# Performance work log

Measured on AMD Instinct MI355X. Metric: run time of the kernel, lower is better.

Reference implementation:

```python
import jax, jax.numpy as jnp
import numpy as np

_R, _C = 64, 64
_N = _R * _C
_SEC_PER_A = 31556926.0
_K = 0.01        # sheet_conductivity
_ALPHA = 1.25    # sheet_flow_exp
_HR = 0.1        # bedrock_step_height
_LR = 2.0        # cavity_spacing
_A = 5e-25       # cavity_closure_coeff
_NEXP = 3        # Glen exponent


def _build_grid():
    idx = np.arange(_N).reshape(_R, _C)
    tail = np.concatenate([idx[:, :-1].ravel(), idx[:-1, :].ravel()]).astype(np.int32)
    head = np.concatenate([idx[:, 1:].ravel(), idx[1:, :].ravel()]).astype(np.int32)
    L = tail.size
    links_at_node = -np.ones((_N, 4), np.int32)
    adj = -np.ones((_N, 4), np.int32)
    cnt = np.zeros(_N, np.int32)
    for l in range(L):
        for a, b in ((tail[l], head[l]), (head[l], tail[l])):
            links_at_node[a, cnt[a]] = l
            adj[a, cnt[a]] = b
            cnt[a] += 1
    r, c = np.divmod(np.arange(_N), _C)
    status = ((r == 0) | (r == _R - 1) | (c == 0) | (c == _C - 1)).astype(np.int32)
    return tail, head, links_at_node, adj, status


def setup_inputs():
    key = jax.random.key(0)
    k = jax.random.split(key, 8)
    tail, head, links_at_node, adj, status = _build_grid()
    L = tail.size
    bedrock = jax.random.uniform(k[0], (_N,), jnp.float32, 0.0, 500.0)
    ice_thk = jax.random.uniform(k[1], (_N,), jnp.float32, 100.0, 1000.0)
    overburden = 917.0 * 9.81 * ice_thk
    base_potential = 1000.0 * 9.81 * bedrock + overburden
    potential = base_potential - 0.3 * overburden + 1e3 * jax.random.normal(k[2], (_N,), jnp.float32)
    sheet_thickness = jax.random.uniform(k[3], (_N,), jnp.float32, 0.01, 0.1)
    sliding_velocity = jax.random.uniform(k[4], (L,), jnp.float32, 10.0, 100.0)
    specific_melt_rate = jax.random.uniform(k[5], (_N,), jnp.float32, 1e-7, 1e-6)
    link_length = jnp.full((L,), 100.0, jnp.float32)
    adj_j = jnp.asarray(adj)
    # mean over ALL 4 slots, padded entries contribute 0 (matches original jnp.mean)
    adj_pot = jnp.mean(jnp.where(adj_j != -1, base_potential[adj_j], 0.0), axis=1)
    inflow = jnp.where(base_potential > adj_pot, 1, -1) * (jnp.asarray(status) > 0)
    return dict(
        base_potential=base_potential,
        overburden_pressure=overburden,
        specific_melt_rate=specific_melt_rate,
        sheet_thickness=sheet_thickness,
        potential=potential,
        sliding_velocity=sliding_velocity,
        link_length=link_length,
        link_tail=jnp.asarray(tail),
        link_head=jnp.asarray(head),
        links_at_node=jnp.asarray(links_at_node),
        inflow_outflow=inflow.astype(jnp.int32),
        dt=3600,
    )


def reference(base_potential, overburden_pressure, specific_melt_rate, sheet_thickness,
              potential, sliding_velocity, link_length, link_tail, link_head,
              links_at_node, inflow_outflow, dt):
    N = base_potential.shape[0]
    t, h = link_tail, link_head
    # --- elliptic operator assembly (per-link, scatter into dense [N,N]) ---
    sheets = 0.5 * (sheet_thickness[t] + sheet_thickness[h])
    inv_grad = jnp.abs((potential[t] - potential[h]) / link_length) ** (-0.5)
    c = -_K * sheets ** _ALPHA * link_length * inv_grad  # symmetric link coefficient (<0)
    dir_row = inflow_outflow == 1  # Dirichlet rows
    ct = jnp.where(dir_row[t], 0.0, c)  # contribution into row tail
    ch = jnp.where(dir_row[h], 0.0, c)  # contribution into row head
    M = (jnp.zeros((N, N), base_potential.dtype)
         .at[t, h].add(ct).at[h, t].add(ch)
         .at[t, t].add(-ct).at[h, h].add(-ch))
    M = jnp.where(dir_row[:, None], jnp.eye(N, dtype=M.dtype), M)
    forcing = jnp.where(dir_row, base_potential - overburden_pressure, specific_melt_rate)
    new_potential = jnp.linalg.solve(M, forcing)
    # --- sheet thickness: map_mean_of_links_to_node then Newton on node-local ODE ---
    valid = links_at_node != -1
    lv = (sliding_velocity / _SEC_PER_A)[links_at_node]  # [N,4]
    sliding = jnp.abs(jnp.sum(jnp.where(valid, lv, 0.0), axis=1)
                      / jnp.maximum(valid.sum(axis=1), 1))
    pressure = base_potential - new_potential
    dtf = jnp.asarray(dt, base_potential.dtype)
    # residual r(h) = h - h0 - dt*(sliding*(HR-h)/LR - A*P^n*h) is LINEAR in h,
    # so Newton converges in one exact step -> closed form:
    new_h = (sheet_thickness + dtf * sliding * _HR / _LR) / (
        1.0 + dtf * (sliding / _LR + _A * pressure ** _NEXP))
    return new_potential, new_h
```

## Files before the change

kernel.cpp:

```cpp
#include <hip/hip_runtime.h>
#include <math.h>


#define NT    512
#define NPT   8
#define NN    4096
#define NC    1024
#define NCC   256
#define CCIT  20
#define MAXIT 40

enum : int { RSHL1 = 0x101, RSHR1 = 0x111,
             ROR8 = 0x128, ROR12 = 0x12C, ROR14 = 0x12E, ROR15 = 0x12F,
             WSHL1 = 0x130, WSHR1 = 0x138 };

template<int CTRL>
__device__ __forceinline__ float dppf(float x) {
    return __int_as_float(__builtin_amdgcn_update_dpp(
        __float_as_int(x), __float_as_int(x), CTRL, 0xF, 0xF, false));
}
template<int CTRL>
__device__ __forceinline__ double dppd(double x) {
    const int lo = __double2loint(x), hi = __double2hiint(x);
    const int l2 = __builtin_amdgcn_update_dpp(lo, lo, CTRL, 0xF, 0xF, false);
    const int h2 = __builtin_amdgcn_update_dpp(hi, hi, CTRL, 0xF, 0xF, false);
    return __hiloint2double(h2, l2);
}
__device__ __forceinline__ void pl16sw(int& a, int& b) {
    asm volatile("s_nop 1\n\tv_permlane16_swap_b32 %0, %1" : "+v"(a), "+v"(b));
}
__device__ __forceinline__ void pl32sw(int& a, int& b) {
    asm volatile("s_nop 1\n\tv_permlane32_swap_b32 %0, %1" : "+v"(a), "+v"(b));
}
__device__ __forceinline__ float shift_dn16(float x, bool inR2) {
    int a = __float_as_int(x), b = __float_as_int(x);
    pl16sw(a, b);
    int g = b, g2 = b;
    pl32sw(g, g2);
    return __int_as_float(inR2 ? g : a);
}
__device__ __forceinline__ float shift_up16(float x, bool inR1) {
    int a = __float_as_int(x), b = __float_as_int(x);
    pl16sw(a, b);
    int d1 = __float_as_int(x), d2 = __float_as_int(x);
    pl32sw(d1, d2);
    int e1 = d2, e2 = d2;
    pl16sw(e1, e2);
    return __int_as_float(inR1 ? e1 : b);
}
__device__ __forceinline__ double dsw32(double x) {
    int lo = __double2loint(x), hi = __double2hiint(x);
    int a = lo, b = lo; pl32sw(a, b);
    int c = hi, d = hi; pl32sw(c, d);
    return __hiloint2double(d, b);
}
__device__ __forceinline__ double dsw16(double x) {
    int lo = __double2loint(x), hi = __double2hiint(x);
    int a = lo, b = lo; pl16sw(a, b);
    int c = hi, d = hi; pl16sw(c, d);
    return __hiloint2double(d, b);
}

__global__ __launch_bounds__(NT, 1)
void sds_solver(const float* __restrict__ base_pot,
                const float* __restrict__ ovb,
                const float* __restrict__ melt,
                const float* __restrict__ sheet,
                const float* __restrict__ pot,
                const float* __restrict__ svel,
                const float* __restrict__ llen,
                const int*   __restrict__ ltail,
                const int*   __restrict__ lhead,
                const int*   __restrict__ lan,
                const int*   __restrict__ inflow,
                const int*   __restrict__ dt_raw,
                float* __restrict__ out,
                int N, int L)
{
    __shared__ __align__(16) float cW[NN], cE[NN], cN[NN], cS[NN];
    __shared__ __align__(16) float FD[NN];
    __shared__ __align__(16) float BNDA[8*128], BNDB[8*128];
    __shared__ __align__(16) float CB[32 + NC + 32];
    __shared__ __align__(16) float CB2[32 + NC + 32];
    __shared__ __align__(16) float EB[32 + NC + 32];
    __shared__ __align__(16) float ccb[NCC];
    __shared__ __align__(16) float cWc_s[NC], cEc_s[NC], cNc_s[NC], cSc_s[NC], dc_s[NC];
    __shared__ double redp[32], redg[16];

    const int tid  = threadIdx.x;
    const int lane = tid & 63;
    const int wid  = tid >> 6;
    const int nb0  = (wid << 9) + lane;

    if (N != NN || L != 8064) return;

    const int dti = dt_raw[0];
    const float as_f = __int_as_float(dti);
    const double dtf = (as_f > 0.5f && as_f < 1.0e12f) ? (double)as_f : (double)dti;

    const float invthf = 0.8f;
    const float c1f = 0.2195122f, c2f = 0.9756098f;
    const float wA = 1.75f;

    {
        const float4 z4 = make_float4(0.f, 0.f, 0.f, 0.f);
        #pragma unroll
        for (int i = tid; i < NN/4; i += NT) {
            ((float4*)cW)[i] = z4; ((float4*)cE)[i] = z4;
            ((float4*)cN)[i] = z4; ((float4*)cS)[i] = z4;
        }
        if (tid < 32) {
            CB[tid]=0.f;  CB[32+NC+tid]=0.f;
            CB2[tid]=0.f; CB2[32+NC+tid]=0.f;
            EB[tid]=0.f;  EB[32+NC+tid]=0.f;
        }
    }
    __syncthreads();

    for (int l = tid; l < 8064; l += NT) {
        int t, h;
        if (l < 4032) {
            const int r = l / 63;
            const int c2 = l - r * 63;
            t = (r << 6) + c2; h = t + 1;
        } else {
            t = l - 4032; h = t + 64;
        }
        const float sheets = 0.5f * (sheet[t] + sheet[h]);
        const float len = llen[l];
        const float grad = fabsf((pot[t] - pot[h]) / len);
        const float c = -0.01f * (sheets * sqrtf(sqrtf(sheets))) * len / sqrtf(grad);
        const bool dt_ = (inflow[t] == 1);
        const bool dh_ = (inflow[h] == 1);
        if (l < 4032) { cE[t] = dt_ ? 0.f : c; cW[h] = dh_ ? 0.f : c; }
        else          { cS[t] = dt_ ? 0.f : c; cN[h] = dh_ ? 0.f : c; }
    }
    __syncthreads();

    float cw[NPT], ce[NPT], cn[NPT], cs[NPT], dgf[NPT], invdf[NPT];
    double bb[NPT], gg[NPT], xv[NPT], rv[NPT];
    bool dirf[NPT];
    auto ldco = [&]() {
        #pragma unroll
        for (int k = 0; k < NPT; ++k) {
            const int n = nb0 + (k << 6);
            cw[k] = cW[n]; ce[k] = cE[n]; cn[k] = cN[n]; cs[k] = cS[n];
        }
    };
    ldco();
    double gsum = 0.0, gcnt = 0.0;
    #pragma unroll
    for (int k = 0; k < NPT; ++k) {
        const int n = nb0 + (k << 6);
        const bool dir = (inflow[n] == 1);
        const double g = (double)base_pot[n] - (double)ovb[n];
        const double d = -((double)cw[k] + (double)ce[k] + (double)cn[k] + (double)cs[k]);
        const double dg = (dir || d == 0.0) ? 1.0 : d;
        dgf[k] = (float)dg; invdf[k] = (float)(1.0 / dg);
        bb[k] = dir ? g : (double)melt[n];
        gg[k] = g; dirf[k] = dir;
        if (dir) { gsum += g; gcnt += 1.0; }
    }
    {
        #pragma unroll
        for (int off = 32; off > 0; off >>= 1) {
            gsum += __shfl_down(gsum, off, 64);
            gcnt += __shfl_down(gcnt, off, 64);
        }
        if (lane == 0) { redg[2*wid] = gsum; redg[2*wid+1] = gcnt; }
        __syncthreads();
        gsum = 0.0; gcnt = 0.0;
        #pragma unroll
        for (int w = 0; w < NT/64; ++w) { gsum += redg[2*w]; gcnt += redg[2*w+1]; }
    }
    const double gmean = gsum / (gcnt > 0.0 ? gcnt : 1.0);

    auto stB = [&](float* B, const float* v) {
        *(float2*)&B[(wid << 7) + (lane << 1)] = make_float2(v[0], v[7]);
    };
    float qf[NPT];
    auto spmvC = [&](const float* B, const float* vr) {
        const float nb = B[(((wid + 7) & 7) << 7) + (lane << 1) + 1];
        const float sb = B[(((wid + 1) & 7) << 7) + (lane << 1) + 0];
        #pragma unroll
        for (int k = 0; k < NPT; ++k) {
            const float wv = dppf<WSHR1>(vr[k]);
            const float ev = dppf<WSHL1>(vr[k]);
            const float nv = k ? vr[k-1] : nb;
            const float sv = (k < NPT-1) ? vr[k+1] : sb;
            qf[k] = dgf[k]*vr[k] + cw[k]*wv + ce[k]*ev + cn[k]*nv + cs[k]*sv;
        }
    };

    {
        float x0r[NPT];
        #pragma unroll
        for (int k = 0; k < NPT; ++k) {
            const float x0f = (float)(dirf[k] ? gg[k] : gmean);
            xv[k] = (double)x0f; x0r[k] = x0f;
        }
        stB(BNDA, x0r); __syncthreads();
        spmvC(BNDA, x0r);
        #pragma unroll
        for (int k = 0; k < NPT; ++k)
            rv[k] = dirf[k] ? 0.0 : (bb[k] - (double)qf[k]);
    }
    __syncthreads();

    {
        #pragma unroll
        for (int k = 0; k < NPT; ++k) {
            const int n = nb0 + (k << 6);
            if (lane != 0  && inflow[n-1]  == 1) cW[n] = 0.f;
            if (lane != 63 && inflow[n+1]  == 1) cE[n] = 0.f;
            if (n >= 64        && inflow[n-64] == 1) cN[n] = 0.f;
            if (n < NN-64      && inflow[n+64] == 1) cS[n] = 0.f;
            FD[n] = dirf[k] ? 0.f : dgf[k];
        }
    }
    __syncthreads();
    ldco();

    #pragma unroll
    for (int q = 0; q < 2; ++q) {
        const int I = 2*tid + q;
        const int R = tid >> 4, C = I & 31;
        const int na = 128*R + 2*C, nbq = na+1, nc_ = na+64, nd = na+65;
        cEc_s[I] = cE[nbq] + cE[nd];
        cWc_s[I] = cW[na] + cW[nc_];
        cNc_s[I] = cN[na] + cN[nbq];
        cSc_s[I] = cS[nc_] + cS[nd];
        const float d = FD[na]+FD[nbq]+FD[nc_]+FD[nd]
                      + 2.0f*(cE[na] + cE[nc_] + cS[na] + cS[nbq]);
        dc_s[I] = (d > 0.f) ? d : 1.0f;
    }
    __syncthreads();

    float cwc[2], cec[2], cnc[2], csc[2], dcr[2], invdc[2];
    {
        float2 t;
        t = *(float2*)&cWc_s[2*tid]; cwc[0]=t.x; cwc[1]=t.y;
        t = *(float2*)&cEc_s[2*tid]; cec[0]=t.x; cec[1]=t.y;
        t = *(float2*)&cNc_s[2*tid]; cnc[0]=t.x; cnc[1]=t.y;
        t = *(float2*)&cSc_s[2*tid]; csc[0]=t.x; csc[1]=t.y;
        t = *(float2*)&dc_s[2*tid];  dcr[0]=t.x; dcr[1]=t.y;
        invdc[0] = 1.0f/dcr[0]; invdc[1] = 1.0f/dcr[1];
    }
    float cwcc[4], cecc[4], cncc[4], cscc[4], dccr[4], invdcc[4];
    if (tid < 64) {
        #pragma unroll
        for (int j = 0; j < 4; ++j) {
            const int Rc = ((tid >> 4) << 2) + j, Cc = tid & 15;
            const int IA = 64*Rc + 2*Cc, IB = IA+1, IC = IA+32, ID = IA+33;
            cecc[j] = cEc_s[IB] + cEc_s[ID];
            cwcc[j] = cWc_s[IA] + cWc_s[IC];
            cncc[j] = cNc_s[IA] + cNc_s[IB];
            cscc[j] = cSc_s[IC] + cSc_s[ID];
            const float d = dc_s[IA]+dc_s[IB]+dc_s[IC]+dc_s[ID]
                          + 2.0f*(cEc_s[IA] + cEc_s[IC] + cSc_s[IA] + cSc_s[IB]);
            dccr[j] = (d > 0.f) ? d : 1.0f;
            invdcc[j] = 1.0f/dccr[j];
        }
    }
    float c1cc[CCIT+1], c2cc[CCIT+1], invthcc;
    {
        const double a = 8e-3, b2 = 2.0;
        const double th = 0.5*(b2+a), de = 0.5*(b2-a), s1 = th/de;
        double rp = 1.0/s1;
        for (int j = 1; j <= CCIT; ++j) {
            const double rj = 1.0/(2.0*s1 - rp);
            c1cc[j] = (float)(rj*rp);
            c2cc[j] = (float)(2.0*rj/de);
            rp = rj;
        }
        invthcc = (float)(1.0/th);
    }
    auto cspmv = [&](const float* B_, float v0, float v1, float& q0, float& q1) {
        const float2 up = *(const float2*)&B_[2*tid];
        const float2 dn = *(const float2*)&B_[64 + 2*tid];
        const float wv = dppf<WSHR1>(v1);
        const float ev = dppf<WSHL1>(v0);
        q0 = dcr[0]*v0 + cwc[0]*wv + cec[0]*v1 + cnc[0]*up.x + csc[0]*dn.x;
        q1 = dcr[1]*v1 + cwc[1]*v0 + cec[1]*ev + cnc[1]*up.y + csc[1]*dn.y;
    };

    double rho_prev = 0.0, pap = 0.0, tol = 0.0;
    double pv[NPT], sv[NPT], rpv[NPT];
    #pragma unroll
    for (int k = 0; k < NPT; ++k) { pv[k]=0.0; sv[k]=0.0; rpv[k]=0.0; }

    for (int it = 0; it < MAXIT; ++it) {
        float f0[NPT], d0[NPT], d1[NPT], zpre[NPT];
        #pragma unroll
        for (int k = 0; k < NPT; ++k) { f0[k] = (float)rv[k] * invdf[k]; d0[k] = f0[k] * invthf; }
        stB(BNDA, d0); __syncthreads();
        spmvC(BNDA, d0);
        #pragma unroll
        for (int k = 0; k < NPT; ++k) {
            const float f1 = f0[k] - qf[k]*invdf[k];
            d1[k] = c1f*d0[k] + c2f*f1;
            zpre[k] = d0[k] + d1[k];
            f0[k] = f1;
        }
        stB(BNDB, d1); __syncthreads();
        spmvC(BNDB, d1);

        float r1[NPT], t2[NPT];
        #pragma unroll
        for (int k = 0; k < NPT; ++k) {
            const float fres = f0[k] - qf[k]*invdf[k];
            r1[k] = dirf[k] ? 0.f : dgf[k]*fres;
        }
        #pragma unroll
        for (int k = 0; k < NPT; ++k) t2[k] = r1[k] + dppf<WSHL1>(r1[k]);
        if ((lane & 1) == 0) {
            #pragma unroll
            for (int j = 0; j < 4; ++j)
                CB2[32 + ((wid << 2) + j)*32 + (lane >> 1)] = t2[2*j] + t2[2*j+1];
        }
        __syncthreads();

        float rc[2], f0c[2], d0c[2], d1c[2], qc0, qc1;
        {
            const float2 rcl = *(const float2*)&CB2[32 + 2*tid];
            rc[0] = rcl.x; rc[1] = rcl.y;
        }
        #pragma unroll
        for (int q = 0; q < 2; ++q) {
            f0c[q] = rc[q] * invdc[q];
            d0c[q] = f0c[q] * invthf;
        }
        *(float2*)&CB[32 + 2*tid] = make_float2(d0c[0], d0c[1]);
        __syncthreads();
        cspmv(CB, d0c[0], d0c[1], qc0, qc1);
        {
            const float f1a = f0c[0] - qc0*invdc[0];
            const float f1b = f0c[1] - qc1*invdc[1];
            d1c[0] = c1f*d0c[0] + c2f*f1a;
            d1c[1] = c1f*d0c[1] + c2f*f1b;
            f0c[0] = f1a; f0c[1] = f1b;
        }
        *(float2*)&CB2[32 + 2*tid] = make_float2(d1c[0], d1c[1]);
        __syncthreads();
        cspmv(CB2, d1c[0], d1c[1], qc0, qc1);
        {
            const float fra = f0c[0] - qc0*invdc[0];
            const float frb = f0c[1] - qc1*invdc[1];
            *(float2*)&CB[32 + 2*tid] = make_float2(dcr[0]*fra, dcr[1]*frb);
        }
        __syncthreads();

        if (tid < 64) {
            const int cc_c  = tid & 15;
            const int cc_rb = tid >> 4;
            const bool inR1 = (cc_rb == 1), inR2 = (cc_rb == 2);
            float fr[4], dr[4], zc[4];
            #pragma unroll
            for (int j = 0; j < 4; ++j) {
                const int IA = (((cc_rb << 2) + j) << 6) + (cc_c << 1);
                const float rcc = CB[32+IA] + CB[32+IA+1] + CB[32+IA+32] + CB[32+IA+33];
                fr[j] = rcc * invdcc[j];
                dr[j] = fr[j] * invthcc;
                zc[j] = dr[j];
            }
            for (int s = 1; s <= CCIT; ++s) {
                const float zN = shift_dn16(dr[3], inR2);
                const float zS = shift_up16(dr[0], inR1);
                float qcc[4];
                #pragma unroll
                for (int j = 0; j < 4; ++j) {
                    const float wj = dppf<RSHR1>(dr[j]);
                    const float ej = dppf<RSHL1>(dr[j]);
                    const float nj = j ? dr[j-1] : zN;
                    const float sj = (j < 3) ? dr[j+1] : zS;
                    qcc[j] = dccr[j]*dr[j] + cwcc[j]*wj + cecc[j]*ej
                           + cncc[j]*nj + cscc[j]*sj;
                }
                #pragma unroll
                for (int j = 0; j < 4; ++j) {
                    fr[j] -= qcc[j] * invdcc[j];
                    dr[j]  = c1cc[s]*dr[j] + c2cc[s]*fr[j];
                    zc[j] += dr[j];
                }
            }
            #pragma unroll
            for (int j = 0; j < 4; ++j)
                ccb[(((cc_rb << 2) + j) << 4) + cc_c] = zc[j];
        }
        __syncthreads();

        const float ecv = wA * ccb[16*(tid >> 5) + (tid & 15)];
        float zmc[2] = { d0c[0] + d1c[0] + ecv, d0c[1] + d1c[1] + ecv };
        *(float2*)&CB2[32 + 2*tid] = make_float2(zmc[0], zmc[1]);
        __syncthreads();
        cspmv(CB2, zmc[0], zmc[1], qc0, qc1);
        float fmc[2] = { (rc[0]-qc0)*invdc[0], (rc[1]-qc1)*invdc[1] };
        float d0p[2] = { fmc[0]*invthf, fmc[1]*invthf };
        *(float2*)&CB[32 + 2*tid] = make_float2(d0p[0], d0p[1]);
        __syncthreads();
        cspmv(CB, d0p[0], d0p[1], qc0, qc1);
        {
            const float f1a = fmc[0] - qc0*invdc[0];
            const float f1b = fmc[1] - qc1*invdc[1];
            const float efa = zmc[0] + c1f*d0p[0] + c2f*f1a + d0p[0];
            const float efb = zmc[1] + c1f*d0p[1] + c2f*f1b + d0p[1];
            *(float2*)&EB[32 + 2*tid] = make_float2(efa, efb);
        }
        __syncthreads();

        float ec[4];
        #pragma unroll
        for (int j = 0; j < 4; ++j)
            ec[j] = EB[32 + ((wid << 2) + j)*32 + (lane >> 1)];
        float zmid[NPT], zf[NPT];
        #pragma unroll
        for (int k = 0; k < NPT; ++k)
            zmid[k] = zpre[k] + (dirf[k] ? 0.f : wA * ec[k >> 1]);
        stB(BNDA, zmid); __syncthreads();
        spmvC(BNDA, zmid);
        float fmid[NPT], d0q[NPT];
        #pragma unroll
        for (int k = 0; k < NPT; ++k) {
            fmid[k] = (float)rv[k]*invdf[k] - qf[k]*invdf[k];
            d0q[k]  = fmid[k] * invthf;
        }
        stB(BNDB, d0q); __syncthreads();
        spmvC(BNDB, d0q);
        #pragma unroll
        for (int k = 0; k < NPT; ++k) {
            const float f1 = fmid[k] - qf[k]*invdf[k];
            zf[k] = zmid[k] + d0q[k] + c1f*d0q[k] + c2f*f1;
        }
        stB(BNDA, zf); __syncthreads();
        spmvC(BNDA, zf);

        double rho_n = 0.0, rzp = 0.0, zw = 0.0, pw = 0.0;
        #pragma unroll
        for (int k = 0; k < NPT; ++k) {
            const double zk = (double)zf[k], wk = (double)qf[k];
            rho_n += rv[k]  * zk;
            rzp   += rpv[k] * zk;
            zw    += zk * wk;
            pw    += pv[k] * wk;
        }
        rho_n += dsw32(rho_n); rzp += dsw32(rzp); zw += dsw32(zw); pw += dsw32(pw);
        rho_n += dsw16(rho_n); rzp += dsw16(rzp); zw += dsw16(zw); pw += dsw16(pw);
        rho_n += dppd<ROR8 >(rho_n); rzp += dppd<ROR8 >(rzp); zw += dppd<ROR8 >(zw); pw += dppd<ROR8 >(pw);
        rho_n += dppd<ROR12>(rho_n); rzp += dppd<ROR12>(rzp); zw += dppd<ROR12>(zw); pw += dppd<ROR12>(pw);
        rho_n += dppd<ROR14>(rho_n); rzp += dppd<ROR14>(rzp); zw += dppd<ROR14>(zw); pw += dppd<ROR14>(pw);
        rho_n += dppd<ROR15>(rho_n); rzp += dppd<ROR15>(rzp); zw += dppd<ROR15>(zw); pw += dppd<ROR15>(pw);
        if (lane == 0) {
            redp[4*wid] = rho_n; redp[4*wid+1] = rzp;
            redp[4*wid+2] = zw;  redp[4*wid+3] = pw;
        }
        __syncthreads();
        rho_n = 0.0; rzp = 0.0; zw = 0.0; pw = 0.0;
        #pragma unroll
        for (int w = 0; w < NT/64; ++w) {
            rho_n += redp[4*w];   rzp += redp[4*w+1];
            zw    += redp[4*w+2]; pw  += redp[4*w+3];
        }

        if (it == 0) {
            tol = rho_n * 1e-3 + 1e-300;
            if (!(rho_n > 0.0)) break;
        } else if (rho_n <= tol || !(rho_n > 0.0)) break;
        const double beta = (it == 0) ? 0.0
                          : fmax(0.0, (rho_n - rzp) / rho_prev);
        pap = zw + beta * (2.0 * pw + beta * pap);
        if (!(pap > 0.0)) break;
        const double alpha = rho_n / pap;
        rho_prev = rho_n;
        #pragma unroll
        for (int k = 0; k < NPT; ++k) {
            rpv[k] = rv[k];
            pv[k] = (double)zf[k] + beta * pv[k];
            sv[k] = (double)qf[k] + beta * sv[k];
            xv[k] += alpha * pv[k];
            rv[k] -= alpha * sv[k];
        }
    }

    #pragma unroll
    for (int k = 0; k < NPT; ++k) {
        const int n = nb0 + (k << 6);
        const int r = (wid << 3) + k, c2 = lane;
        const double x = dirf[k] ? gg[k] : xv[k];

        const int hb = r * 63 + c2;
        float sva = 0.0f; int cnt = 0;
        if (c2 > 0)  { sva += svel[hb - 1];       cnt++; }
        if (c2 < 63) { sva += svel[hb];           cnt++; }
        if (r  > 0)  { sva += svel[4032 + n - 64]; cnt++; }
        if (r  < 63) { sva += svel[4032 + n];      cnt++; }
        const double sliding =
            fabs((double)sva / 31556926.0 / (double)(cnt > 0 ? cnt : 1));
        const double P   = (double)base_pot[n] - x;
        const double num = (double)sheet[n] + dtf * sliding * 0.1 / 2.0;
        const double den = 1.0 + dtf * (sliding / 2.0 + 5e-25 * P * P * P);
        out[n]      = (float)x;
        out[NN + n] = (float)(num / den);
    }
}

extern "C" void kernel_launch(void* const* d_in, const int* in_sizes, int n_in,
                              void* d_out, int out_size, void* d_ws, size_t ws_size,
                              hipStream_t stream) {
    const float* base_pot = (const float*)d_in[0];
    const float* ovb      = (const float*)d_in[1];
    const float* melt     = (const float*)d_in[2];
    const float* sheet    = (const float*)d_in[3];
    const float* pot      = (const float*)d_in[4];
    const float* svel     = (const float*)d_in[5];
    const float* llen     = (const float*)d_in[6];
    const int*   ltail    = (const int*)d_in[7];
    const int*   lhead    = (const int*)d_in[8];
    const int*   lan      = (const int*)d_in[9];
    const int*   inflow   = (const int*)d_in[10];
    const int*   dt_raw   = (const int*)d_in[11];
    float* out = (float*)d_out;
    const int N = in_sizes[0];
    const int L = in_sizes[5];

    hipLaunchKernelGGL(sds_solver, dim3(1), dim3(NT), 0, stream,
                       base_pot, ovb, melt, sheet, pot, svel, llen,
                       ltail, lhead, lan, inflow, dt_raw, out, N, L);
}
```

Baseline: 131.0 us.

## Use ghost-row halos to remove barriers from smoother SpMVs in PCG loop

Each wave now keeps coefficients and residuals for two halo rows above and below its strip. The first two polynomial-smoother SpMVs are computed redundantly on the extended strip, so their shared-memory boundary exchanges and __syncthreads are no longer needed. Halo residuals are updated from neighbor q values published through a new shared buffer each iteration. The trade is extra redundant arithmetic and register pressure (12-row arrays plus extra doubles) for fewer block-wide barriers per iteration.

```diff
diff --git a/kernel.cpp b/kernel.cpp
--- a/kernel.cpp
+++ b/kernel.cpp
@@ -4,6 +4,8 @@
 
 #define NT    512
 #define NPT   8
+#define GD    2
+#define NE    12
 #define NN    4096
 #define NC    1024
 #define NCC   256
@@ -80,6 +82,7 @@
     __shared__ __align__(16) float cW[NN], cE[NN], cN[NN], cS[NN];
     __shared__ __align__(16) float FD[NN];
     __shared__ __align__(16) float BNDA[8*128], BNDB[8*128];
+    __shared__ __align__(16) float QB[32*64];
     __shared__ __align__(16) float CB[32 + NC + 32];
     __shared__ __align__(16) float CB2[32 + NC + 32];
     __shared__ __align__(16) float EB[32 + NC + 32];
@@ -90,7 +93,6 @@
     const int tid  = threadIdx.x;
     const int lane = tid & 63;
     const int wid  = tid >> 6;
-    const int nb0  = (wid << 9) + lane;
 
     if (N != NN || L != 8064) return;
 
@@ -137,31 +139,44 @@
     }
     __syncthreads();
 
-    float cw[NPT], ce[NPT], cn[NPT], cs[NPT], dgf[NPT], invdf[NPT];
-    double bb[NPT], gg[NPT], xv[NPT], rv[NPT];
+    float cwE[NE], ceE[NE], cnE[NE], csE[NE], dgE[NE], invdE[NE];
+    double xv[NPT], rv[NPT];
+    double rga[GD], sga[GD], rgb[GD], sgb[GD];
     bool dirf[NPT];
-    auto ldco = [&]() {
-        #pragma unroll
-        for (int k = 0; k < NPT; ++k) {
-            const int n = nb0 + (k << 6);
-            cw[k] = cW[n]; ce[k] = cE[n]; cn[k] = cN[n]; cs[k] = cS[n];
+
+    auto ldcoE = [&]() {
+        #pragma unroll
+        for (int e = 0; e < NE; ++e) {
+            const int gr = (wid << 3) - GD + e;
+            const bool val = (gr >= 0) && (gr < 64);
+            const int n = ((val ? gr : 0) << 6) + lane;
+            cwE[e] = val ? cW[n] : 0.f;
+            ceE[e] = val ? cE[n] : 0.f;
+            cnE[e] = val ? cN[n] : 0.f;
+            csE[e] = val ? cS[n] : 0.f;
         }
     };
-    ldco();
+    ldcoE();
     double gsum = 0.0, gcnt = 0.0;
-    #pragma unroll
-    for (int k = 0; k < NPT; ++k) {
-        const int n = nb0 + (k << 6);
-        const bool dir = (inflow[n] == 1);
-        const double g = (double)base_pot[n] - (double)ovb[n];
-        const double d = -((double)cw[k] + (double)ce[k] + (double)cn[k] + (double)cs[k]);
-        const double dg = (dir || d == 0.0) ? 1.0 : d;
-        dgf[k] = (float)dg; invdf[k] = (float)(1.0 / dg);
-        bb[k] = dir ? g : (double)melt[n];
-        gg[k] = g; dirf[k] = dir;
-        if (dir) { gsum += g; gcnt += 1.0; }
-    }
     {
+        #pragma unroll
+        for (int e = 0; e < NE; ++e) {
+            const int gr = (wid << 3) - GD + e;
+            const bool val = (gr >= 0) && (gr < 64);
+            const int n = ((val ? gr : 0) << 6) + lane;
+            const bool dir = val && (inflow[n] == 1);
+            const double d = -((double)cwE[e] + (double)ceE[e] + (double)cnE[e] + (double)csE[e]);
+            const double dg = (dir || d == 0.0) ? 1.0 : d;
+            dgE[e] = (float)dg; invdE[e] = (float)(1.0 / dg);
+            if (e >= GD && e < GD + NPT) {
+                const int k = e - GD;
+                dirf[k] = dir;
+                if (dir) {
+                    const double g = (double)base_pot[n] - (double)ovb[n];
+                    gsum += g; gcnt += 1.0;
+                }
+            }
+        }
         #pragma unroll
         for (int off = 32; off > 0; off >>= 1) {
             gsum += __shfl_down(gsum, off, 64);
@@ -175,51 +190,66 @@
     }
     const double gmean = gsum / (gcnt > 0.0 ? gcnt : 1.0);
 
-    auto stB = [&](float* B, const float* v) {
-        *(float2*)&B[(wid << 7) + (lane << 1)] = make_float2(v[0], v[7]);
-    };
-    float qf[NPT];
-    auto spmvC = [&](const float* B, const float* vr) {
-        const float nb = B[(((wid + 7) & 7) << 7) + (lane << 1) + 1];
-        const float sb = B[(((wid + 1) & 7) << 7) + (lane << 1) + 0];
-        #pragma unroll
-        for (int k = 0; k < NPT; ++k) {
-            const float wv = dppf<WSHR1>(vr[k]);
-            const float ev = dppf<WSHL1>(vr[k]);
-            const float nv = k ? vr[k-1] : nb;
-            const float sv = (k < NPT-1) ? vr[k+1] : sb;
-            qf[k] = dgf[k]*vr[k] + cw[k]*wv + ce[k]*ev + cn[k]*nv + cs[k]*sv;
-        }
-    };
-
     {
-        float x0r[NPT];
-        #pragma unroll
-        for (int k = 0; k < NPT; ++k) {
-            const float x0f = (float)(dirf[k] ? gg[k] : gmean);
-            xv[k] = (double)x0f; x0r[k] = x0f;
-        }
-        stB(BNDA, x0r); __syncthreads();
-        spmvC(BNDA, x0r);
-        #pragma unroll
-        for (int k = 0; k < NPT; ++k)
-            rv[k] = dirf[k] ? 0.0 : (bb[k] - (double)qf[k]);
+        auto x0at = [&](int gr) -> float {
+            if (gr < 0 || gr >= 64) return 0.f;
+            const int n = (gr << 6) + lane;
+            const bool dir = (inflow[n] == 1);
+            const double g = (double)base_pot[n] - (double)ovb[n];
+            return (float)(dir ? g : gmean);
+        };
+        float x0E[NE];
+        #pragma unroll
+        for (int e = 0; e < NE; ++e) x0E[e] = x0at((wid << 3) - GD + e);
+        const float x0m = x0at((wid << 3) - GD - 1);
+        const float x0p = x0at((wid << 3) - GD + NE);
+        float qx[NE];
+        #pragma unroll
+        for (int e = 0; e < NE; ++e) {
+            const float wv = dppf<WSHR1>(x0E[e]);
+            const float ev = dppf<WSHL1>(x0E[e]);
+            const float nv = e ? x0E[e-1] : x0m;
+            const float sv_ = (e < NE-1) ? x0E[e+1] : x0p;
+            qx[e] = dgE[e]*x0E[e] + cwE[e]*wv + ceE[e]*ev + cnE[e]*nv + csE[e]*sv_;
+        }
+        #pragma unroll
+        for (int k = 0; k < NPT; ++k) {
+            const int n = (((wid << 3) + k) << 6) + lane;
+            xv[k] = (double)x0E[k + GD];
+            const double bbk = dirf[k]
+                ? ((double)base_pot[n] - (double)ovb[n]) : (double)melt[n];
+            rv[k] = dirf[k] ? 0.0 : (bbk - (double)qx[k + GD]);
+        }
+        #pragma unroll
+        for (int j = 0; j < GD; ++j) {
+            const int gra = (wid << 3) - GD + j;
+            const int grb = (wid << 3) + NPT + j;
+            const bool va = (gra >= 0);
+            const bool vb = (grb < 64);
+            const int na = ((va ? gra : 0) << 6) + lane;
+            const int nb = ((vb ? grb : 0) << 6) + lane;
+            const bool da = va && (inflow[na] == 1);
+            const bool db = vb && (inflow[nb] == 1);
+            rga[j] = (!va || da) ? 0.0 : ((double)melt[na] - (double)qx[j]);
+            rgb[j] = (!vb || db) ? 0.0 : ((double)melt[nb] - (double)qx[NE-GD+j]);
+            sga[j] = 0.0; sgb[j] = 0.0;
+        }
     }
     __syncthreads();
 
     {
         #pragma unroll
         for (int k = 0; k < NPT; ++k) {
-            const int n = nb0 + (k << 6);
+            const int n = (((wid << 3) + k) << 6) + lane;
             if (lane != 0  && inflow[n-1]  == 1) cW[n] = 0.f;
             if (lane != 63 && inflow[n+1]  == 1) cE[n] = 0.f;
             if (n >= 64        && inflow[n-64] == 1) cN[n] = 0.f;
             if (n < NN-64      && inflow[n+64] == 1) cS[n] = 0.f;
-            FD[n] = dirf[k] ? 0.f : dgf[k];
+            FD[n] = dirf[k] ? 0.f : dgE[k + GD];
         }
     }
     __syncthreads();
-    ldco();
+    ldcoE();
 
     #pragma unroll
     for (int q = 0; q < 2; ++q) {
@@ -284,39 +314,70 @@
         q1 = dcr[1]*v1 + cwc[1]*v0 + cec[1]*ev + cnc[1]*up.y + csc[1]*dn.y;
     };
 
+    auto stB = [&](float* B, const float* v) {
+        *(float2*)&B[(wid << 7) + (lane << 1)] = make_float2(v[0], v[7]);
+    };
+    float qf[NPT];
+    auto spmvC = [&](const float* B, const float* vr) {
+        const float nb = B[(((wid + 7) & 7) << 7) + (lane << 1) + 1];
+        const float sb = B[(((wid + 1) & 7) << 7) + (lane << 1) + 0];
+        #pragma unroll
+        for (int k = 0; k < NPT; ++k) {
+            const float wv = dppf<WSHR1>(vr[k]);
+            const float ev = dppf<WSHL1>(vr[k]);
+            const float nv = k ? vr[k-1] : nb;
+            const float sv_ = (k < NPT-1) ? vr[k+1] : sb;
+            qf[k] = dgE[k+GD]*vr[k] + cwE[k+GD]*wv + ceE[k+GD]*ev
+                  + cnE[k+GD]*nv + csE[k+GD]*sv_;
+        }
+    };
+
     double rho_prev = 0.0, pap = 0.0, tol = 0.0;
     double pv[NPT], sv[NPT], rpv[NPT];
     #pragma unroll
     for (int k = 0; k < NPT; ++k) { pv[k]=0.0; sv[k]=0.0; rpv[k]=0.0; }
 
     for (int it = 0; it < MAXIT; ++it) {
-        float f0[NPT], d0[NPT], d1[NPT], zpre[NPT];
-        #pragma unroll
-        for (int k = 0; k < NPT; ++k) { f0[k] = (float)rv[k] * invdf[k]; d0[k] = f0[k] * invthf; }
-        stB(BNDA, d0); __syncthreads();
-        spmvC(BNDA, d0);
-        #pragma unroll
-        for (int k = 0; k < NPT; ++k) {
-            const float f1 = f0[k] - qf[k]*invdf[k];
-            d1[k] = c1f*d0[k] + c2f*f1;
-            zpre[k] = d0[k] + d1[k];
-            f0[k] = f1;
-        }
-        stB(BNDB, d1); __syncthreads();
-        spmvC(BNDB, d1);
-
-        float r1[NPT], t2[NPT];
-        #pragma unroll
-        for (int k = 0; k < NPT; ++k) {
-            const float fres = f0[k] - qf[k]*invdf[k];
-            r1[k] = dirf[k] ? 0.f : dgf[k]*fres;
-        }
-        #pragma unroll
-        for (int k = 0; k < NPT; ++k) t2[k] = r1[k] + dppf<WSHL1>(r1[k]);
-        if ((lane & 1) == 0) {
+        float f0E[NE], d0E[NE], d1E[NE], zpre[NPT];
+        #pragma unroll
+        for (int e = 0; e < NE; ++e) {
+            const float rvf = (e < GD) ? (float)rga[e]
+                            : (e >= GD+NPT) ? (float)rgb[e-GD-NPT]
+                            : (float)rv[e-GD];
+            f0E[e] = rvf * invdE[e];
+            d0E[e] = f0E[e] * invthf;
+        }
+        #pragma unroll
+        for (int e = 1; e <= NE-2; ++e) {
+            const float wv = dppf<WSHR1>(d0E[e]);
+            const float ev = dppf<WSHL1>(d0E[e]);
+            const float q = dgE[e]*d0E[e] + cwE[e]*wv + ceE[e]*ev
+                          + cnE[e]*d0E[e-1] + csE[e]*d0E[e+1];
+            const float f1 = f0E[e] - q*invdE[e];
+            d1E[e] = c1f*d0E[e] + c2f*f1;
+            f0E[e] = f1;
+            if (e >= GD && e < GD+NPT) zpre[e-GD] = d0E[e] + d1E[e];
+        }
+        float r1[NPT];
+        #pragma unroll
+        for (int k = 0; k < NPT; ++k) {
+            const int e = k + GD;
+            const float wv = dppf<WSHR1>(d1E[e]);
+            const float ev = dppf<WSHL1>(d1E[e]);
+            const float q = dgE[e]*d1E[e] + cwE[e]*wv + ceE[e]*ev
+                          + cnE[e]*d1E[e-1] + csE[e]*d1E[e+1];
+            const float fres = f0E[e] - q*invdE[e];
+            r1[k] = dirf[k] ? 0.f : dgE[e]*fres;
+        }
+        {
+            float t2[NPT];
             #pragma unroll
-            for (int j = 0; j < 4; ++j)
-                CB2[32 + ((wid << 2) + j)*32 + (lane >> 1)] = t2[2*j] + t2[2*j+1];
+            for (int k = 0; k < NPT; ++k) t2[k] = r1[k] + dppf<WSHL1>(r1[k]);
+            if ((lane & 1) == 0) {
+                #pragma unroll
+                for (int j = 0; j < 4; ++j)
+                    CB2[32 + ((wid << 2) + j)*32 + (lane >> 1)] = t2[2*j] + t2[2*j+1];
+            }
         }
         __syncthreads();
 
@@ -421,14 +482,14 @@
         float fmid[NPT], d0q[NPT];
         #pragma unroll
         for (int k = 0; k < NPT; ++k) {
-            fmid[k] = (float)rv[k]*invdf[k] - qf[k]*invdf[k];
+            fmid[k] = (float)rv[k]*invdE[k+GD] - qf[k]*invdE[k+GD];
             d0q[k]  = fmid[k] * invthf;
         }
         stB(BNDB, d0q); __syncthreads();
         spmvC(BNDB, d0q);
         #pragma unroll
         for (int k = 0; k < NPT; ++k) {
-            const float f1 = fmid[k] - qf[k]*invdf[k];
+            const float f1 = fmid[k] - qf[k]*invdE[k+GD];
             zf[k] = zmid[k] + d0q[k] + c1f*d0q[k] + c2f*f1;
         }
         stB(BNDA, zf); __syncthreads();
@@ -449,6 +510,10 @@
         rho_n += dppd<ROR12>(rho_n); rzp += dppd<ROR12>(rzp); zw += dppd<ROR12>(zw); pw += dppd<ROR12>(pw);
         rho_n += dppd<ROR14>(rho_n); rzp += dppd<ROR14>(rzp); zw += dppd<ROR14>(zw); pw += dppd<ROR14>(pw);
         rho_n += dppd<ROR15>(rho_n); rzp += dppd<ROR15>(rzp); zw += dppd<ROR15>(zw); pw += dppd<ROR15>(pw);
+        QB[((wid << 2) + 0)*64 + lane] = qf[0];
+        QB[((wid << 2) + 1)*64 + lane] = qf[1];
+        QB[((wid << 2) + 2)*64 + lane] = qf[6];
+        QB[((wid << 2) + 3)*64 + lane] = qf[7];
         if (lane == 0) {
             redp[4*wid] = rho_n; redp[4*wid+1] = rzp;
             redp[4*wid+2] = zw;  redp[4*wid+3] = pw;
@@ -479,13 +544,23 @@
             xv[k] += alpha * pv[k];
             rv[k] -= alpha * sv[k];
         }
+        #pragma unroll
+        for (int j = 0; j < GD; ++j) {
+            const float qga = (wid > 0) ? QB[(((wid-1) << 2) + 2 + j)*64 + lane] : 0.f;
+            sga[j] = (double)qga + beta * sga[j];
+            rga[j] -= alpha * sga[j];
+            const float qgb = (wid < 7) ? QB[(((wid+1) << 2) + 0 + j)*64 + lane] : 0.f;
+            sgb[j] = (double)qgb + beta * sgb[j];
+            rgb[j] -= alpha * sgb[j];
+        }
     }
 
     #pragma unroll
     for (int k = 0; k < NPT; ++k) {
-        const int n = nb0 + (k << 6);
+        const int n = (((wid << 3) + k) << 6) + lane;
         const int r = (wid << 3) + k, c2 = lane;
-        const double x = dirf[k] ? gg[k] : xv[k];
+        const double g = (double)base_pot[n] - (double)ovb[n];
+        const double x = dirf[k] ? g : xv[k];
 
         const int hb = r * 63 + c2;
         float sva = 0.0f; int cnt = 0;
```

Measured after the change: 155.8 us. 1.19x slower.
